# Kernel optimization log

Measured on AMD Instinct MI355X. Metric: run time of the kernel, lower is better.

Reference implementation:

```python
import jax, jax.numpy as jnp
from jax import lax
import numpy as np

B, T, I, H, STEPS = 512, 256, 64, 512, 10


def setup_inputs() -> dict:
    key = jax.random.key(0)
    ks = jax.random.split(key, 11)
    k = 1.0 / np.sqrt(H)  # PyTorch default init bound
    u = lambda kk, shape: jax.random.uniform(kk, shape, jnp.float32, -k, k)
    return dict(
        x=jax.random.normal(ks[0], (B, T, I), jnp.float32),
        W_ih0=u(ks[1], (4 * H, I)), W_hh0=u(ks[2], (4 * H, H)),
        b_ih0=u(ks[3], (4 * H,)), b_hh0=u(ks[4], (4 * H,)),
        W_ih1=u(ks[5], (4 * H, H)), W_hh1=u(ks[6], (4 * H, H)),
        b_ih1=u(ks[7], (4 * H,)), b_hh1=u(ks[8], (4 * H,)),
        W_lin=u(ks[9], (I, H)), b_lin=u(ks[10], (I,)),
        future_steps=STEPS,
    )


def _cell(x_t, h, c, W_ih, W_hh, b):
    # PyTorch LSTM gate order: i, f, g, o
    gates = x_t @ W_ih.T + h @ W_hh.T + b
    i, f, g, o = jnp.split(gates, 4, axis=-1)
    c_new = jax.nn.sigmoid(f) * c + jax.nn.sigmoid(i) * jnp.tanh(g)
    h_new = jax.nn.sigmoid(o) * jnp.tanh(c_new)
    return h_new, c_new


def _layer_scan(xs, W_ih, W_hh, b):
    # xs: [B, T, D] -> outputs [B, T, H], final (h, c)
    Bsz, Hd = xs.shape[0], W_hh.shape[1]
    h0 = jnp.zeros((Bsz, Hd), xs.dtype)

    def step(carry, x_t):
        h, c = _cell(x_t, carry[0], carry[1], W_ih, W_hh, b)
        return (h, c), h

    (h, c), ys = lax.scan(step, (h0, h0), jnp.swapaxes(xs, 0, 1))
    return jnp.swapaxes(ys, 0, 1), (h, c)


def reference(x, W_ih0, W_hh0, b_ih0, b_hh0, W_ih1, W_hh1, b_ih1, b_hh1, W_lin, b_lin, future_steps):
    b0 = b_ih0 + b_hh0
    b1 = b_ih1 + b_hh1
    # encoder pass over the conditioning sequence
    ys0, (h0f, c0f) = _layer_scan(x, W_ih0, W_hh0, b0)
    _, (h1f, c1f) = _layer_scan(ys0, W_ih1, W_hh1, b1)
    inp = x[:, -1, :]

    def dec_step(carry, _):
        cur, h0, c0, h1, c1 = carry
        h0, c0 = _cell(cur, h0, c0, W_ih0, W_hh0, b0)
        h1, c1 = _cell(h0, h1, c1, W_ih1, W_hh1, b1)
        out = h1 @ W_lin.T + b_lin  # [B, I]
        return (out, h0, c0, h1, c1), out

    _, outs = lax.scan(dec_step, (inp, h0f, c0f, h1f, c1f), None, length=future_steps)
    return jnp.swapaxes(outs, 0, 1)  # [B, future_steps, I]
```

## Files before the change

### kernel.cpp

```cpp
#include <hip/hip_runtime.h>
#include <hip/hip_bf16.h>
#include <stdint.h>

#define BSZ 512
#define TT  256
#define IIN 64
#define HH  512
#define G4  2048
#define NSTEPS 10

typedef short bf16x8 __attribute__((ext_vector_type(8)));
typedef float f32x4  __attribute__((ext_vector_type(4)));

__device__ __forceinline__ unsigned short f2bf(float f){
  union { float f; uint32_t u; } v; v.f = f;
  uint32_t u = v.u;
  uint32_t r = (u + 0x7fffu + ((u >> 16) & 1u)) >> 16;
  return (unsigned short)r;
}
__device__ __forceinline__ float bf2f(unsigned short h){
  union { uint32_t u; float f; } v; v.u = ((uint32_t)h) << 16;
  return v.f;
}
__device__ __forceinline__ float sigf(float x){ return 1.0f/(1.0f+__expf(-x)); }
__device__ __forceinline__ float tanhfast(float x){ return 1.0f - 2.0f/(__expf(2.0f*x)+1.0f); }

__device__ void cell_body(int wg,
    const float* __restrict__ A1, long a1s, int k1c,
    const unsigned short* __restrict__ W1h, const unsigned short* __restrict__ W1l,
    const float* __restrict__ A2,
    const unsigned short* __restrict__ W2h, const unsigned short* __restrict__ W2l,
    const float* __restrict__ bias,
    float* __restrict__ cbuf, float* __restrict__ hout)
{
  __shared__ unsigned short sAh[64*40];
  __shared__ unsigned short sAl[64*40];
  __shared__ unsigned short sBh[64*40];
  __shared__ unsigned short sBl[64*40];
  __shared__ float sG[4*64*16];

  const int tid = threadIdx.x;
  const int btile = wg >> 5;
  const int ct = wg & 31;
  const int b0 = btile * 64;
  const int j0 = ct * 16;
  const int g  = tid >> 6;
  const int l  = tid & 63;
  const int lr = l & 15;
  const int lk = (l >> 4) * 8;

  const int r  = tid >> 2;
  const int c8 = (tid & 3) * 8;
  const int w1len = k1c * 32;
  const int qn = (r >> 4) * 512 + j0 + (r & 15);

  f32x4 acc[4];
  {
    float bv = bias[g*512 + j0 + lr];
    f32x4 ini = {bv, bv, bv, bv};
    #pragma unroll
    for (int m = 0; m < 4; ++m) acc[m] = ini;
  }

  const int nch = k1c + 16;
  for (int kc = 0; kc < nch; ++kc){
    const float* asrc;
    if (kc < k1c) asrc = A1 + (long)(b0 + r) * a1s + kc*32 + c8;
    else          asrc = A2 + ((long)(b0 + r) << 9) + ((kc - k1c)*32 + c8);
    f32x4 v0 = *(const f32x4*)asrc;
    f32x4 v1 = *(const f32x4*)(asrc + 4);
    union { unsigned short u[8]; bf16x8 v; } hi, lo;
    #pragma unroll
    for (int i = 0; i < 4; ++i){
      float f = v0[i]; unsigned short h = f2bf(f);
      hi.u[i] = h; lo.u[i] = f2bf(f - bf2f(h));
    }
    #pragma unroll
    for (int i = 0; i < 4; ++i){
      float f = v1[i]; unsigned short h = f2bf(f);
      hi.u[4+i] = h; lo.u[4+i] = f2bf(f - bf2f(h));
    }
    *(bf16x8*)&sAh[r*40 + c8] = hi.v;
    *(bf16x8*)&sAl[r*40 + c8] = lo.v;

    {
      long woff; const unsigned short *wh, *wl;
      if (kc < k1c){ woff = (long)qn * w1len + kc*32 + c8; wh = W1h; wl = W1l; }
      else         { woff = ((long)qn << 9) + (kc - k1c)*32 + c8; wh = W2h; wl = W2l; }
      *(bf16x8*)&sBh[r*40 + c8] = *(const bf16x8*)&wh[woff];
      *(bf16x8*)&sBl[r*40 + c8] = *(const bf16x8*)&wl[woff];
    }
    __syncthreads();

    bf16x8 bh = *(const bf16x8*)&sBh[(g*16 + lr)*40 + lk];
    bf16x8 bl = *(const bf16x8*)&sBl[(g*16 + lr)*40 + lk];
    #pragma unroll
    for (int m = 0; m < 4; ++m){
      bf16x8 ah = *(const bf16x8*)&sAh[(m*16 + lr)*40 + lk];
      bf16x8 al = *(const bf16x8*)&sAl[(m*16 + lr)*40 + lk];
      acc[m] = __builtin_amdgcn_mfma_f32_16x16x32_bf16(ah, bh, acc[m], 0, 0, 0);
      acc[m] = __builtin_amdgcn_mfma_f32_16x16x32_bf16(ah, bl, acc[m], 0, 0, 0);
      acc[m] = __builtin_amdgcn_mfma_f32_16x16x32_bf16(al, bh, acc[m], 0, 0, 0);
    }
    __syncthreads();
  }

  #pragma unroll
  for (int m = 0; m < 4; ++m){
    int rowb = m*16 + (l >> 4)*4;
    #pragma unroll
    for (int q = 0; q < 4; ++q)
      sG[(g*64 + rowb + q)*16 + lr] = acc[m][q];
  }
  __syncthreads();
  {
    int e0 = tid * 4;
    int row = e0 >> 4;
    int col0 = e0 & 15;
    #pragma unroll
    for (int q = 0; q < 4; ++q){
      int col = col0 + q;
      float gi = sG[(0*64+row)*16 + col];
      float gf = sG[(1*64+row)*16 + col];
      float gg = sG[(2*64+row)*16 + col];
      float go = sG[(3*64+row)*16 + col];
      long idx = ((long)(b0+row) << 9) + j0 + col;
      float cold = cbuf[idx];
      float cn = sigf(gf)*cold + sigf(gi)*tanhfast(gg);
      cbuf[idx] = cn;
      hout[idx] = sigf(go)*tanhfast(cn);
    }
  }
}

__global__ __launch_bounds__(256, 2)
void enc_step(const float* __restrict__ x,
              const unsigned short* Wih0h, const unsigned short* Wih0l,
              const unsigned short* Whh0h, const unsigned short* Whh0l,
              const float* b0v,
              const unsigned short* Wih1h, const unsigned short* Wih1l,
              const unsigned short* Whh1h, const unsigned short* Whh1l,
              const float* b1v,
              float* h0a, float* h0b, float* h1a, float* h1b,
              float* c0, float* c1, int s)
{
  int role = blockIdx.x >> 8;
  int wg   = blockIdx.x & 255;
  int rp = (s + 1) & 1;
  int wp = s & 1;
  const float* h0r = rp ? h0b : h0a;
  float*       h0w = wp ? h0b : h0a;
  const float* h1r = rp ? h1b : h1a;
  float*       h1w = wp ? h1b : h1a;

  if (role == 0){
    if (s >= TT) return;
    cell_body(wg, x + (long)s*IIN, (long)TT*IIN, 2,
              Wih0h, Wih0l, h0r, Whh0h, Whh0l, b0v, c0, h0w);
  } else {
    if (s < 1) return;
    cell_body(wg, h0r, (long)HH, 16,
              Wih1h, Wih1l, h1r, Whh1h, Whh1l, b1v, c1, h1w);
  }
}

__global__ __launch_bounds__(256, 2)
void dec_cell(const float* A1, long a1s, int k1c,
              const unsigned short* W1h, const unsigned short* W1l,
              const float* A2,
              const unsigned short* W2h, const unsigned short* W2l,
              const float* bias, float* cbuf, float* hout)
{
  cell_body(blockIdx.x, A1, a1s, k1c, W1h, W1l, A2, W2h, W2l, bias, cbuf, hout);
}

__global__ __launch_bounds__(256)
void lin_kernel(const float* __restrict__ h1, const float* __restrict__ Wlin,
                const float* __restrict__ blin, float* __restrict__ out)
{
  int gt = blockIdx.x * 256 + threadIdx.x;
  int b = gt >> 6;
  int i = gt & 63;
  const float* hr = h1 + ((long)b << 9);
  const float* wr = Wlin + ((long)i << 9);
  float s = 0.f;
  #pragma unroll 4
  for (int k = 0; k < HH; k += 4){
    f32x4 hv = *(const f32x4*)(hr + k);
    f32x4 wv = *(const f32x4*)(wr + k);
    s += hv[0]*wv[0] + hv[1]*wv[1] + hv[2]*wv[2] + hv[3]*wv[3];
  }
  out[(long)b * (NSTEPS*IIN) + i] = s + blin[i];
}

__global__ void bias_kernel(const float* a, const float* b, float* o){
  int i = blockIdx.x * 256 + threadIdx.x;
  if (i < G4) o[i] = a[i] + b[i];
}
__global__ void split_kernel(const float* __restrict__ src,
                             unsigned short* __restrict__ hi,
                             unsigned short* __restrict__ lo, int n){
  int i = blockIdx.x * 256 + threadIdx.x;
  if (i < n){
    float f = src[i];
    unsigned short h = f2bf(f);
    hi[i] = h;
    lo[i] = f2bf(f - bf2f(h));
  }
}

extern "C" void kernel_launch(void* const* d_in, const int* in_sizes, int n_in,
                              void* d_out, int out_size, void* d_ws, size_t ws_size,
                              hipStream_t stream)
{
  const float* x     = (const float*)d_in[0];
  const float* W_ih0 = (const float*)d_in[1];
  const float* W_hh0 = (const float*)d_in[2];
  const float* b_ih0 = (const float*)d_in[3];
  const float* b_hh0 = (const float*)d_in[4];
  const float* W_ih1 = (const float*)d_in[5];
  const float* W_hh1 = (const float*)d_in[6];
  const float* b_ih1 = (const float*)d_in[7];
  const float* b_hh1 = (const float*)d_in[8];
  const float* W_lin = (const float*)d_in[9];
  const float* b_lin = (const float*)d_in[10];
  float* out = (float*)d_out;

  char* ws = (char*)d_ws;
  size_t off = 0;
  auto alloc = [&](size_t bytes){ size_t o = off; off += (bytes + 255) & ~(size_t)255; return o; };

  float* b0v = (float*)(ws + alloc(G4*4));
  float* b1v = (float*)(ws + alloc(G4*4));
  unsigned short* Wih0h = (unsigned short*)(ws + alloc((size_t)G4*IIN*2));
  unsigned short* Wih0l = (unsigned short*)(ws + alloc((size_t)G4*IIN*2));
  unsigned short* Whh0h = (unsigned short*)(ws + alloc((size_t)G4*HH*2));
  unsigned short* Whh0l = (unsigned short*)(ws + alloc((size_t)G4*HH*2));
  unsigned short* Wih1h = (unsigned short*)(ws + alloc((size_t)G4*HH*2));
  unsigned short* Wih1l = (unsigned short*)(ws + alloc((size_t)G4*HH*2));
  unsigned short* Whh1h = (unsigned short*)(ws + alloc((size_t)G4*HH*2));
  unsigned short* Whh1l = (unsigned short*)(ws + alloc((size_t)G4*HH*2));
  const size_t BH = (size_t)BSZ * HH;
  float* states = (float*)(ws + alloc(6 * BH * 4));
  float* h0a = states;
  float* h0b = states + BH;
  float* h1a = states + 2*BH;
  float* h1b = states + 3*BH;
  float* c0  = states + 4*BH;
  float* c1  = states + 5*BH;

  bias_kernel<<<(G4+255)/256, 256, 0, stream>>>(b_ih0, b_hh0, b0v);
  bias_kernel<<<(G4+255)/256, 256, 0, stream>>>(b_ih1, b_hh1, b1v);
  {
    int n0 = G4*IIN, n1 = G4*HH;
    split_kernel<<<(n0+255)/256, 256, 0, stream>>>(W_ih0, Wih0h, Wih0l, n0);
    split_kernel<<<(n1+255)/256, 256, 0, stream>>>(W_hh0, Whh0h, Whh0l, n1);
    split_kernel<<<(n1+255)/256, 256, 0, stream>>>(W_ih1, Wih1h, Wih1l, n1);
    split_kernel<<<(n1+255)/256, 256, 0, stream>>>(W_hh1, Whh1h, Whh1l, n1);
  }
  hipMemsetAsync(states, 0, 6 * BH * 4, stream);

  for (int s = 0; s <= TT; ++s){
    enc_step<<<512, 256, 0, stream>>>(x,
        Wih0h, Wih0l, Whh0h, Whh0l, b0v,
        Wih1h, Wih1l, Whh1h, Whh1l, b1v,
        h0a, h0b, h1a, h1b, c0, c1, s);
  }

  float* h0_cur = h0b; float* h0_alt = h0a;
  float* h1_cur = h1a; float* h1_alt = h1b;

  for (int s = 0; s < NSTEPS; ++s){
    const float* cur; long cs;
    if (s == 0){ cur = x + (long)(TT-1)*IIN; cs = (long)TT*IIN; }
    else       { cur = out + (long)(s-1)*IIN; cs = (long)NSTEPS*IIN; }

    dec_cell<<<256, 256, 0, stream>>>(cur, cs, 2, Wih0h, Wih0l,
                                      h0_cur, Whh0h, Whh0l, b0v, c0, h0_alt);
    { float* t = h0_cur; h0_cur = h0_alt; h0_alt = t; }

    dec_cell<<<256, 256, 0, stream>>>(h0_cur, (long)HH, 16, Wih1h, Wih1l,
                                      h1_cur, Whh1h, Whh1l, b1v, c1, h1_alt);
    { float* t = h1_cur; h1_cur = h1_alt; h1_alt = t; }

    lin_kernel<<<128, 256, 0, stream>>>(h1_cur, W_lin, b_lin, out + (long)s*IIN);
  }
}
```

Before: 9.033 ms.

## Fuse LSTM steps into persistent cooperative kernel with pre-split bf16 states and packed weights

Replaces about 287 per-step kernel launches with one cooperative persistent kernel that uses grid.sync between timesteps, and keeps launch-per-step kernels as a fallback. Hidden states are stored already split into hi/lo bf16 halves, so the per-step float-to-bf16 conversion of activations goes away. Weights are repacked per column tile with input and recurrent K concatenated, and the K loop now uses 64-wide chunks with an XOR-swizzled LDS layout and a K-split across waves reduced through LDS. Grid syncs across 512 blocks add their own overhead, and the rewrite changes indexing in many places.

```diff
diff --git a/kernel.cpp b/kernel.cpp
--- a/kernel.cpp
+++ b/kernel.cpp
@@ -1,6 +1,9 @@
 #include <hip/hip_runtime.h>
 #include <hip/hip_bf16.h>
+#include <hip/hip_cooperative_groups.h>
 #include <stdint.h>
+
+namespace cg = cooperative_groups;
 
 #define BSZ 512
 #define TT  256
@@ -9,204 +12,328 @@
 #define G4  2048
 #define NSTEPS 10
 
+typedef unsigned short ushort_t;
 typedef short bf16x8 __attribute__((ext_vector_type(8)));
 typedef float f32x4  __attribute__((ext_vector_type(4)));
 
-__device__ __forceinline__ unsigned short f2bf(float f){
+static constexpr size_t N0W = (size_t)G4 * 576;
+static constexpr size_t NTW = N0W + (size_t)G4 * 1024;
+
+__device__ __forceinline__ ushort_t f2bf(float f){
   union { float f; uint32_t u; } v; v.f = f;
   uint32_t u = v.u;
-  uint32_t r = (u + 0x7fffu + ((u >> 16) & 1u)) >> 16;
-  return (unsigned short)r;
-}
-__device__ __forceinline__ float bf2f(unsigned short h){
+  return (ushort_t)((u + 0x7fffu + ((u >> 16) & 1u)) >> 16);
+}
+__device__ __forceinline__ float bf2f(ushort_t h){
   union { uint32_t u; float f; } v; v.u = ((uint32_t)h) << 16;
   return v.f;
 }
+__device__ __forceinline__ void split2(float f, ushort_t& h, ushort_t& l){
+  h = f2bf(f); l = f2bf(f - bf2f(h));
+}
 __device__ __forceinline__ float sigf(float x){ return 1.0f/(1.0f+__expf(-x)); }
 __device__ __forceinline__ float tanhfast(float x){ return 1.0f - 2.0f/(__expf(2.0f*x)+1.0f); }
 
-__device__ void cell_body(int wg,
-    const float* __restrict__ A1, long a1s, int k1c,
-    const unsigned short* __restrict__ W1h, const unsigned short* __restrict__ W1l,
-    const float* __restrict__ A2,
-    const unsigned short* __restrict__ W2h, const unsigned short* __restrict__ W2l,
-    const float* __restrict__ bias,
-    float* __restrict__ cbuf, float* __restrict__ hout)
+struct KP {
+  const float* x;
+  const ushort_t *Wph, *Wpl;
+  const float *b0v, *b1v;
+  const float *Wlin, *blin;
+  ushort_t *h0h0, *h0h1, *h0l0, *h0l1;
+  ushort_t *h1h0, *h1h1, *h1l0, *h1l1;
+  float *c0, *c1;
+  ushort_t *outh, *outl;
+  float* out;
+};
+
+__device__ __forceinline__ void cell_tile(ushort_t* lds,
+  int b0, int j0,
+  const float* a1f, const ushort_t* a1h, const ushort_t* a1l, int a1s, int k1,
+  const ushort_t* a2h, const ushort_t* a2l,
+  const ushort_t* wpbh, const ushort_t* wpbl, int K, int nrounds,
+  const float* bias, float* cbuf, ushort_t* houth, ushort_t* houtl)
 {
-  __shared__ unsigned short sAh[64*40];
-  __shared__ unsigned short sAl[64*40];
-  __shared__ unsigned short sBh[64*40];
-  __shared__ unsigned short sBl[64*40];
-  __shared__ float sG[4*64*16];
-
   const int tid = threadIdx.x;
-  const int btile = wg >> 5;
-  const int ct = wg & 31;
-  const int b0 = btile * 64;
-  const int j0 = ct * 16;
-  const int g  = tid >> 6;
+  const int w  = tid >> 6;
   const int l  = tid & 63;
+  const int km = w & 1;
+  const int mh = w >> 1;
   const int lr = l & 15;
-  const int lk = (l >> 4) * 8;
-
-  const int r  = tid >> 2;
-  const int c8 = (tid & 3) * 8;
-  const int w1len = k1c * 32;
-  const int qn = (r >> 4) * 512 + j0 + (r & 15);
-
-  f32x4 acc[4];
-  {
-    float bv = bias[g*512 + j0 + lr];
-    f32x4 ini = {bv, bv, bv, bv};
-    #pragma unroll
-    for (int m = 0; m < 4; ++m) acc[m] = ini;
-  }
-
-  const int nch = k1c + 16;
-  for (int kc = 0; kc < nch; ++kc){
-    const float* asrc;
-    if (kc < k1c) asrc = A1 + (long)(b0 + r) * a1s + kc*32 + c8;
-    else          asrc = A2 + ((long)(b0 + r) << 9) + ((kc - k1c)*32 + c8);
-    f32x4 v0 = *(const f32x4*)asrc;
-    f32x4 v1 = *(const f32x4*)(asrc + 4);
-    union { unsigned short u[8]; bf16x8 v; } hi, lo;
-    #pragma unroll
-    for (int i = 0; i < 4; ++i){
-      float f = v0[i]; unsigned short h = f2bf(f);
-      hi.u[i] = h; lo.u[i] = f2bf(f - bf2f(h));
-    }
-    #pragma unroll
-    for (int i = 0; i < 4; ++i){
-      float f = v1[i]; unsigned short h = f2bf(f);
-      hi.u[4+i] = h; lo.u[4+i] = f2bf(f - bf2f(h));
-    }
-    *(bf16x8*)&sAh[r*40 + c8] = hi.v;
-    *(bf16x8*)&sAl[r*40 + c8] = lo.v;
-
-    {
-      long woff; const unsigned short *wh, *wl;
-      if (kc < k1c){ woff = (long)qn * w1len + kc*32 + c8; wh = W1h; wl = W1l; }
-      else         { woff = ((long)qn << 9) + (kc - k1c)*32 + c8; wh = W2h; wl = W2l; }
-      *(bf16x8*)&sBh[r*40 + c8] = *(const bf16x8*)&wh[woff];
-      *(bf16x8*)&sBl[r*40 + c8] = *(const bf16x8*)&wl[woff];
+  const int kh = l >> 4;
+
+  f32x4 acc[2][4];
+  #pragma unroll
+  for (int mm=0; mm<2; ++mm)
+    #pragma unroll
+    for (int nn=0; nn<4; ++nn)
+      acc[mm][nn] = (f32x4){0.f,0.f,0.f,0.f};
+
+  ushort_t* sAh = lds;
+  ushort_t* sAl = lds + 4096;
+  ushort_t* sBh = lds + 8192;
+  ushort_t* sBl = lds + 12288;
+
+  for (int r = 0; r < nrounds; ++r){
+    #pragma unroll
+    for (int q = 0; q < 2; ++q){
+      int u   = q*256 + tid;
+      int row = u >> 3;
+      int j   = u & 7;
+      int jl  = j ^ (row & 7);
+      int klog = r*64 + jl*8;
+      int didx = u * 8;
+      bf16x8 hv, lv;
+      if (klog < k1){
+        if (a1f){
+          const float* ps = a1f + (size_t)(b0+row)*a1s + klog;
+          f32x4 u0 = *(const f32x4*)ps;
+          f32x4 u1 = *(const f32x4*)(ps+4);
+          union { ushort_t us[8]; bf16x8 v; } H, L;
+          #pragma unroll
+          for (int jj=0;jj<4;++jj) split2(u0[jj], H.us[jj],   L.us[jj]);
+          #pragma unroll
+          for (int jj=0;jj<4;++jj) split2(u1[jj], H.us[4+jj], L.us[4+jj]);
+          hv = H.v; lv = L.v;
+        } else {
+          hv = *(const bf16x8*)&a1h[(size_t)(b0+row)*a1s + klog];
+          lv = *(const bf16x8*)&a1l[(size_t)(b0+row)*a1s + klog];
+        }
+      } else {
+        int kk = klog - k1;
+        hv = *(const bf16x8*)&a2h[(size_t)((b0+row)<<9) + kk];
+        lv = *(const bf16x8*)&a2l[(size_t)((b0+row)<<9) + kk];
+      }
+      *(bf16x8*)&sAh[didx] = hv;
+      *(bf16x8*)&sAl[didx] = lv;
+      size_t bsrc = (size_t)row*K + klog;
+      *(bf16x8*)&sBh[didx] = *(const bf16x8*)&wpbh[bsrc];
+      *(bf16x8*)&sBl[didx] = *(const bf16x8*)&wpbl[bsrc];
     }
     __syncthreads();
-
-    bf16x8 bh = *(const bf16x8*)&sBh[(g*16 + lr)*40 + lk];
-    bf16x8 bl = *(const bf16x8*)&sBl[(g*16 + lr)*40 + lk];
-    #pragma unroll
-    for (int m = 0; m < 4; ++m){
-      bf16x8 ah = *(const bf16x8*)&sAh[(m*16 + lr)*40 + lk];
-      bf16x8 al = *(const bf16x8*)&sAl[(m*16 + lr)*40 + lk];
-      acc[m] = __builtin_amdgcn_mfma_f32_16x16x32_bf16(ah, bh, acc[m], 0, 0, 0);
-      acc[m] = __builtin_amdgcn_mfma_f32_16x16x32_bf16(ah, bl, acc[m], 0, 0, 0);
-      acc[m] = __builtin_amdgcn_mfma_f32_16x16x32_bf16(al, bh, acc[m], 0, 0, 0);
+    const int ju = km*4 + kh;
+    bf16x8 ah[2], al[2];
+    #pragma unroll
+    for (int mm=0; mm<2; ++mm){
+      int rowa = (mh*2+mm)*16 + lr;
+      int idx = (rowa*8 + (ju ^ (rowa&7)))*8;
+      ah[mm] = *(bf16x8*)&sAh[idx];
+      al[mm] = *(bf16x8*)&sAl[idx];
+    }
+    #pragma unroll
+    for (int nn=0; nn<4; ++nn){
+      int rowb = nn*16 + lr;
+      int idx = (rowb*8 + (ju ^ (rowb&7)))*8;
+      bf16x8 bh = *(bf16x8*)&sBh[idx];
+      bf16x8 bl = *(bf16x8*)&sBl[idx];
+      #pragma unroll
+      for (int mm=0; mm<2; ++mm){
+        acc[mm][nn] = __builtin_amdgcn_mfma_f32_16x16x32_bf16(ah[mm], bh, acc[mm][nn],0,0,0);
+        acc[mm][nn] = __builtin_amdgcn_mfma_f32_16x16x32_bf16(ah[mm], bl, acc[mm][nn],0,0,0);
+        acc[mm][nn] = __builtin_amdgcn_mfma_f32_16x16x32_bf16(al[mm], bh, acc[mm][nn],0,0,0);
+      }
     }
     __syncthreads();
   }
 
-  #pragma unroll
-  for (int m = 0; m < 4; ++m){
-    int rowb = m*16 + (l >> 4)*4;
-    #pragma unroll
-    for (int q = 0; q < 4; ++q)
-      sG[(g*64 + rowb + q)*16 + lr] = acc[m][q];
+  float* sR = (float*)lds;
+  if (km == 1){
+    #pragma unroll
+    for (int mm=0; mm<2; ++mm)
+      #pragma unroll
+      for (int nn=0; nn<4; ++nn){
+        int c = mm*4 + nn;
+        *(f32x4*)&sR[mh*2048 + l*32 + (c ^ (l&7))*4] = acc[mm][nn];
+      }
   }
   __syncthreads();
-  {
-    int e0 = tid * 4;
-    int row = e0 >> 4;
-    int col0 = e0 & 15;
-    #pragma unroll
-    for (int q = 0; q < 4; ++q){
-      int col = col0 + q;
-      float gi = sG[(0*64+row)*16 + col];
-      float gf = sG[(1*64+row)*16 + col];
-      float gg = sG[(2*64+row)*16 + col];
-      float go = sG[(3*64+row)*16 + col];
-      long idx = ((long)(b0+row) << 9) + j0 + col;
-      float cold = cbuf[idx];
-      float cn = sigf(gf)*cold + sigf(gi)*tanhfast(gg);
-      cbuf[idx] = cn;
-      hout[idx] = sigf(go)*tanhfast(cn);
+  if (km == 0){
+    #pragma unroll
+    for (int mm=0; mm<2; ++mm)
+      #pragma unroll
+      for (int nn=0; nn<4; ++nn){
+        int c = mm*4 + nn;
+        acc[mm][nn] += *(f32x4*)&sR[mh*2048 + l*32 + (c ^ (l&7))*4];
+      }
+    float bi = bias[       j0 + lr];
+    float bf = bias[ 512 + j0 + lr];
+    float bg = bias[1024 + j0 + lr];
+    float bo = bias[1536 + j0 + lr];
+    #pragma unroll
+    for (int mm=0; mm<2; ++mm){
+      #pragma unroll
+      for (int q=0; q<4; ++q){
+        int row = (mh*2+mm)*16 + kh*4 + q;
+        float gi = acc[mm][0][q] + bi;
+        float gf = acc[mm][1][q] + bf;
+        float gg = acc[mm][2][q] + bg;
+        float go = acc[mm][3][q] + bo;
+        size_t gidx = (size_t)((b0+row)<<9) + j0 + lr;
+        float cold = cbuf[gidx];
+        float cn = sigf(gf)*cold + sigf(gi)*tanhfast(gg);
+        cbuf[gidx] = cn;
+        float hval = sigf(go)*tanhfast(cn);
+        ushort_t hh2, hl2; split2(hval, hh2, hl2);
+        houth[gidx] = hh2; houtl[gidx] = hl2;
+      }
     }
   }
-}
-
-__global__ __launch_bounds__(256, 2)
-void enc_step(const float* __restrict__ x,
-              const unsigned short* Wih0h, const unsigned short* Wih0l,
-              const unsigned short* Whh0h, const unsigned short* Whh0l,
-              const float* b0v,
-              const unsigned short* Wih1h, const unsigned short* Wih1l,
-              const unsigned short* Whh1h, const unsigned short* Whh1l,
-              const float* b1v,
-              float* h0a, float* h0b, float* h1a, float* h1b,
-              float* c0, float* c1, int s)
-{
-  int role = blockIdx.x >> 8;
-  int wg   = blockIdx.x & 255;
-  int rp = (s + 1) & 1;
-  int wp = s & 1;
-  const float* h0r = rp ? h0b : h0a;
-  float*       h0w = wp ? h0b : h0a;
-  const float* h1r = rp ? h1b : h1a;
-  float*       h1w = wp ? h1b : h1a;
-
+  __syncthreads();
+}
+
+__device__ __forceinline__ void do_enc(const KP& p, ushort_t* lds, int bid, int s){
+  const int role = bid >> 8;
+  const int tile = bid & 255;
+  const int m = tile >> 5, nt = tile & 31;
+  const int b0 = m*64, j0 = nt*16;
+  ushort_t* h0h[2] = { p.h0h0, p.h0h1 };
+  ushort_t* h0l[2] = { p.h0l0, p.h0l1 };
+  ushort_t* h1h[2] = { p.h1h0, p.h1h1 };
+  ushort_t* h1l[2] = { p.h1l0, p.h1l1 };
   if (role == 0){
     if (s >= TT) return;
-    cell_body(wg, x + (long)s*IIN, (long)TT*IIN, 2,
-              Wih0h, Wih0l, h0r, Whh0h, Whh0l, b0v, c0, h0w);
+    const int t = s;
+    cell_tile(lds, b0, j0,
+      p.x + (size_t)t*IIN, nullptr, nullptr, TT*IIN, 64,
+      h0h[(t+1)&1], h0l[(t+1)&1],
+      p.Wph + (size_t)nt*64*576, p.Wpl + (size_t)nt*64*576, 576, 9,
+      p.b0v, p.c0, h0h[t&1], h0l[t&1]);
   } else {
     if (s < 1) return;
-    cell_body(wg, h0r, (long)HH, 16,
-              Wih1h, Wih1l, h1r, Whh1h, Whh1l, b1v, c1, h1w);
-  }
+    const int t = s-1;
+    cell_tile(lds, b0, j0,
+      nullptr, h0h[t&1], h0l[t&1], 512, 512,
+      h1h[(t+1)&1], h1l[(t+1)&1],
+      p.Wph + N0W + (size_t)nt*64*1024, p.Wpl + N0W + (size_t)nt*64*1024, 1024, 16,
+      p.b1v, p.c1, h1h[t&1], h1l[t&1]);
+  }
+}
+
+__device__ __forceinline__ void do_dec0(const KP& p, ushort_t* lds, int tile, int d, int p0){
+  const int m = tile >> 5, nt = tile & 31;
+  const int b0 = m*64, j0 = nt*16;
+  ushort_t* h0h[2] = { p.h0h0, p.h0h1 };
+  ushort_t* h0l[2] = { p.h0l0, p.h0l1 };
+  const ushort_t* w0h = p.Wph + (size_t)nt*64*576;
+  const ushort_t* w0l = p.Wpl + (size_t)nt*64*576;
+  if (d == 0)
+    cell_tile(lds, b0, j0,
+      p.x + (size_t)(TT-1)*IIN, nullptr, nullptr, TT*IIN, 64,
+      h0h[p0], h0l[p0], w0h, w0l, 576, 9,
+      p.b0v, p.c0, h0h[1-p0], h0l[1-p0]);
+  else
+    cell_tile(lds, b0, j0,
+      nullptr, p.outh, p.outl, 64, 64,
+      h0h[p0], h0l[p0], w0h, w0l, 576, 9,
+      p.b0v, p.c0, h0h[1-p0], h0l[1-p0]);
+}
+
+__device__ __forceinline__ void do_dec1(const KP& p, ushort_t* lds, int tile, int p0, int p1){
+  const int m = tile >> 5, nt = tile & 31;
+  const int b0 = m*64, j0 = nt*16;
+  ushort_t* h0h[2] = { p.h0h0, p.h0h1 };
+  ushort_t* h0l[2] = { p.h0l0, p.h0l1 };
+  ushort_t* h1h[2] = { p.h1h0, p.h1h1 };
+  ushort_t* h1l[2] = { p.h1l0, p.h1l1 };
+  cell_tile(lds, b0, j0,
+    nullptr, h0h[1-p0], h0l[1-p0], 512, 512,
+    h1h[p1], h1l[p1],
+    p.Wph + N0W + (size_t)nt*64*1024, p.Wpl + N0W + (size_t)nt*64*1024, 1024, 16,
+    p.b1v, p.c1, h1h[1-p1], h1l[1-p1]);
+}
+
+__device__ __forceinline__ void do_lin(const KP& p, int bid, int d, int p1){
+  ushort_t* h1h[2] = { p.h1h0, p.h1h1 };
+  ushort_t* h1l[2] = { p.h1l0, p.h1l1 };
+  const ushort_t* hhp = h1h[1-p1];
+  const ushort_t* hlp = h1l[1-p1];
+  int row = bid*4 + (threadIdx.x >> 6);
+  int i   = threadIdx.x & 63;
+  const float* wr = p.Wlin + (size_t)i*512;
+  float ssum = 0.f;
+  for (int k = 0; k < 512; k += 8){
+    bf16x8 vh = *(const bf16x8*)&hhp[(size_t)(row<<9)+k];
+    bf16x8 vl = *(const bf16x8*)&hlp[(size_t)(row<<9)+k];
+    #pragma unroll
+    for (int jj=0;jj<8;++jj)
+      ssum += (bf2f((ushort_t)vh[jj]) + bf2f((ushort_t)vl[jj])) * wr[k+jj];
+  }
+  ssum += p.blin[i];
+  p.out[(size_t)row*(NSTEPS*IIN) + d*IIN + i] = ssum;
+  ushort_t oh, ol; split2(ssum, oh, ol);
+  p.outh[row*64 + i] = oh;
+  p.outl[row*64 + i] = ol;
 }
 
 __global__ __launch_bounds__(256, 2)
-void dec_cell(const float* A1, long a1s, int k1c,
-              const unsigned short* W1h, const unsigned short* W1l,
-              const float* A2,
-              const unsigned short* W2h, const unsigned short* W2l,
-              const float* bias, float* cbuf, float* hout)
+void lstm_persist(KP p)
 {
-  cell_body(blockIdx.x, A1, a1s, k1c, W1h, W1l, A2, W2h, W2l, bias, cbuf, hout);
-}
-
+  const int bid = blockIdx.x;
+  __shared__ ushort_t lds[16384];
+  cg::grid_group grid = cg::this_grid();
+
+  for (int s = 0; s <= TT; ++s){
+    do_enc(p, lds, bid, s);
+    grid.sync();
+  }
+  int p0 = 1, p1 = 1;
+  for (int d = 0; d < NSTEPS; ++d){
+    if (bid < 256) do_dec0(p, lds, bid, d, p0);
+    grid.sync();
+    if (bid >= 256) do_dec1(p, lds, bid & 255, p0, p1);
+    grid.sync();
+    if (bid < 128) do_lin(p, bid, d, p1);
+    grid.sync();
+    p0 ^= 1; p1 ^= 1;
+  }
+}
+
+__global__ __launch_bounds__(256, 2)
+void fb_enc(KP p, int s){
+  __shared__ ushort_t lds[16384];
+  do_enc(p, lds, blockIdx.x, s);
+}
+__global__ __launch_bounds__(256, 2)
+void fb_dec0(KP p, int d, int p0){
+  __shared__ ushort_t lds[16384];
+  do_dec0(p, lds, blockIdx.x, d, p0);
+}
+__global__ __launch_bounds__(256, 2)
+void fb_dec1(KP p, int p0, int p1){
+  __shared__ ushort_t lds[16384];
+  do_dec1(p, lds, blockIdx.x, p0, p1);
+}
 __global__ __launch_bounds__(256)
-void lin_kernel(const float* __restrict__ h1, const float* __restrict__ Wlin,
-                const float* __restrict__ blin, float* __restrict__ out)
-{
-  int gt = blockIdx.x * 256 + threadIdx.x;
-  int b = gt >> 6;
-  int i = gt & 63;
-  const float* hr = h1 + ((long)b << 9);
-  const float* wr = Wlin + ((long)i << 9);
-  float s = 0.f;
-  #pragma unroll 4
-  for (int k = 0; k < HH; k += 4){
-    f32x4 hv = *(const f32x4*)(hr + k);
-    f32x4 wv = *(const f32x4*)(wr + k);
-    s += hv[0]*wv[0] + hv[1]*wv[1] + hv[2]*wv[2] + hv[3]*wv[3];
-  }
-  out[(long)b * (NSTEPS*IIN) + i] = s + blin[i];
+void fb_lin(KP p, int d, int p1){
+  do_lin(p, blockIdx.x, d, p1);
 }
 
 __global__ void bias_kernel(const float* a, const float* b, float* o){
   int i = blockIdx.x * 256 + threadIdx.x;
   if (i < G4) o[i] = a[i] + b[i];
 }
-__global__ void split_kernel(const float* __restrict__ src,
-                             unsigned short* __restrict__ hi,
-                             unsigned short* __restrict__ lo, int n){
-  int i = blockIdx.x * 256 + threadIdx.x;
-  if (i < n){
-    float f = src[i];
-    unsigned short h = f2bf(f);
-    hi[i] = h;
-    lo[i] = f2bf(f - bf2f(h));
-  }
+
+__global__ void prep_w(const float* __restrict__ Wih0, const float* __restrict__ Whh0,
+                       const float* __restrict__ Wih1, const float* __restrict__ Whh1,
+                       ushort_t* __restrict__ Wph, ushort_t* __restrict__ Wpl)
+{
+  size_t i = (size_t)blockIdx.x*256 + threadIdx.x;
+  if (i >= NTW) return;
+  float val;
+  if (i < N0W){
+    size_t e = i;
+    int nt = (int)(e / (64*576)); int rem = (int)(e % (64*576));
+    int cl = rem / 576; int k = rem % 576;
+    int grow = (cl>>4)*512 + nt*16 + (cl&15);
+    val = (k < 64) ? Wih0[(size_t)grow*64 + k] : Whh0[(size_t)grow*512 + (k-64)];
+  } else {
+    size_t e = i - N0W;
+    int nt = (int)(e >> 16); int rem = (int)(e & 65535);
+    int cl = rem >> 10; int k = rem & 1023;
+    int grow = (cl>>4)*512 + nt*16 + (cl&15);
+    val = (k < 512) ? Wih1[(size_t)grow*512 + k] : Whh1[(size_t)grow*512 + (k-512)];
+  }
+  ushort_t h, lo2; split2(val, h, lo2);
+  Wph[i] = h; Wpl[i] = lo2;
 }
 
 extern "C" void kernel_launch(void* const* d_in, const int* in_sizes, int n_in,
@@ -224,7 +351,6 @@
   const float* b_hh1 = (const float*)d_in[8];
   const float* W_lin = (const float*)d_in[9];
   const float* b_lin = (const float*)d_in[10];
-  float* out = (float*)d_out;
 
   char* ws = (char*)d_ws;
   size_t off = 0;
@@ -232,57 +358,47 @@
 
   float* b0v = (float*)(ws + alloc(G4*4));
   float* b1v = (float*)(ws + alloc(G4*4));
-  unsigned short* Wih0h = (unsigned short*)(ws + alloc((size_t)G4*IIN*2));
-  unsigned short* Wih0l = (unsigned short*)(ws + alloc((size_t)G4*IIN*2));
-  unsigned short* Whh0h = (unsigned short*)(ws + alloc((size_t)G4*HH*2));
-  unsigned short* Whh0l = (unsigned short*)(ws + alloc((size_t)G4*HH*2));
-  unsigned short* Wih1h = (unsigned short*)(ws + alloc((size_t)G4*HH*2));
-  unsigned short* Wih1l = (unsigned short*)(ws + alloc((size_t)G4*HH*2));
-  unsigned short* Whh1h = (unsigned short*)(ws + alloc((size_t)G4*HH*2));
-  unsigned short* Whh1l = (unsigned short*)(ws + alloc((size_t)G4*HH*2));
+  ushort_t* Wph = (ushort_t*)(ws + alloc(NTW*2));
+  ushort_t* Wpl = (ushort_t*)(ws + alloc(NTW*2));
+
   const size_t BH = (size_t)BSZ * HH;
-  float* states = (float*)(ws + alloc(6 * BH * 4));
-  float* h0a = states;
-  float* h0b = states + BH;
-  float* h1a = states + 2*BH;
-  float* h1b = states + 3*BH;
-  float* c0  = states + 4*BH;
-  float* c1  = states + 5*BH;
+  size_t statesBytes = 8*BH*2 + 2*BH*4 + 2*(size_t)BSZ*IIN*2;
+  char* states = ws + alloc(statesBytes);
+  ushort_t* hbufs = (ushort_t*)states;
+  ushort_t* h0h0 = hbufs;          ushort_t* h0h1 = hbufs + BH;
+  ushort_t* h0l0 = hbufs + 2*BH;   ushort_t* h0l1 = hbufs + 3*BH;
+  ushort_t* h1h0 = hbufs + 4*BH;   ushort_t* h1h1 = hbufs + 5*BH;
+  ushort_t* h1l0 = hbufs + 6*BH;   ushort_t* h1l1 = hbufs + 7*BH;
+  float* c0 = (float*)(states + 8*BH*2);
+  float* c1 = c0 + BH;
+  ushort_t* outh = (ushort_t*)(states + 8*BH*2 + 2*BH*4);
+  ushort_t* outl = outh + (size_t)BSZ*IIN;
 
   bias_kernel<<<(G4+255)/256, 256, 0, stream>>>(b_ih0, b_hh0, b0v);
   bias_kernel<<<(G4+255)/256, 256, 0, stream>>>(b_ih1, b_hh1, b1v);
-  {
-    int n0 = G4*IIN, n1 = G4*HH;
-    split_kernel<<<(n0+255)/256, 256, 0, stream>>>(W_ih0, Wih0h, Wih0l, n0);
-    split_kernel<<<(n1+255)/256, 256, 0, stream>>>(W_hh0, Whh0h, Whh0l, n1);
-    split_kernel<<<(n1+255)/256, 256, 0, stream>>>(W_ih1, Wih1h, Wih1l, n1);
-    split_kernel<<<(n1+255)/256, 256, 0, stream>>>(W_hh1, Whh1h, Whh1l, n1);
-  }
-  hipMemsetAsync(states, 0, 6 * BH * 4, stream);
-
-  for (int s = 0; s <= TT; ++s){
-    enc_step<<<512, 256, 0, stream>>>(x,
-        Wih0h, Wih0l, Whh0h, Whh0l, b0v,
-        Wih1h, Wih1l, Whh1h, Whh1l, b1v,
-        h0a, h0b, h1a, h1b, c0, c1, s);
-  }
-
-  float* h0_cur = h0b; float* h0_alt = h0a;
-  float* h1_cur = h1a; float* h1_alt = h1b;
-
-  for (int s = 0; s < NSTEPS; ++s){
-    const float* cur; long cs;
-    if (s == 0){ cur = x + (long)(TT-1)*IIN; cs = (long)TT*IIN; }
-    else       { cur = out + (long)(s-1)*IIN; cs = (long)NSTEPS*IIN; }
-
-    dec_cell<<<256, 256, 0, stream>>>(cur, cs, 2, Wih0h, Wih0l,
-                                      h0_cur, Whh0h, Whh0l, b0v, c0, h0_alt);
-    { float* t = h0_cur; h0_cur = h0_alt; h0_alt = t; }
-
-    dec_cell<<<256, 256, 0, stream>>>(h0_cur, (long)HH, 16, Wih1h, Wih1l,
-                                      h1_cur, Whh1h, Whh1l, b1v, c1, h1_alt);
-    { float* t = h1_cur; h1_cur = h1_alt; h1_alt = t; }
-
-    lin_kernel<<<128, 256, 0, stream>>>(h1_cur, W_lin, b_lin, out + (long)s*IIN);
-  }
-}
+  prep_w<<<(int)((NTW+255)/256), 256, 0, stream>>>(W_ih0, W_hh0, W_ih1, W_hh1, Wph, Wpl);
+  hipMemsetAsync(states, 0, statesBytes, stream);
+
+  KP kp;
+  kp.x = x; kp.Wph = Wph; kp.Wpl = Wpl; kp.b0v = b0v; kp.b1v = b1v;
+  kp.Wlin = W_lin; kp.blin = b_lin;
+  kp.h0h0 = h0h0; kp.h0h1 = h0h1; kp.h0l0 = h0l0; kp.h0l1 = h0l1;
+  kp.h1h0 = h1h0; kp.h1h1 = h1h1; kp.h1l0 = h1l0; kp.h1l1 = h1l1;
+  kp.c0 = c0; kp.c1 = c1; kp.outh = outh; kp.outl = outl;
+  kp.out = (float*)d_out;
+
+  void* kargs[] = { &kp };
+  hipError_t ce = hipLaunchCooperativeKernel((void*)lstm_persist,
+                                             dim3(512), dim3(256), kargs, 0, stream);
+  if (ce != hipSuccess){
+    for (int s = 0; s <= TT; ++s)
+      fb_enc<<<512, 256, 0, stream>>>(kp, s);
+    int p0 = 1, p1 = 1;
+    for (int d = 0; d < NSTEPS; ++d){
+      fb_dec0<<<256, 256, 0, stream>>>(kp, d, p0);
+      fb_dec1<<<256, 256, 0, stream>>>(kp, p0, p1);
+      fb_lin<<<128, 256, 0, stream>>>(kp, d, p1);
+      p0 ^= 1; p1 ^= 1;
+    }
+  }
+}
```

After: 21.85 ms. 2.42x slower.
